# Kernel optimization log

Hardware: AMD Instinct MI355X
Metric: run time of the kernel (lower is better)

## Reference

```python
import jax, jax.numpy as jnp
import numpy as np

IMAGE_SIZE = 1024      # config.model.image_size
DOWNSIZING = 64        # PromptGetter default grid downsizing
THRESHOLD = 0.65       # default_threshold_target
NEG = -1e9             # stand-in for -inf that keeps argmax well-defined


def setup_inputs() -> dict:
    key = jax.random.key(0)
    k1, k2 = jax.random.split(key)
    image_embeddings = jax.random.normal(k1, (1, 256, 64, 64), dtype=jnp.float32)
    reference_feats = jax.random.normal(k2, (64, 1, 256), dtype=jnp.float32)
    # reference feats are L2-normalized masked features in the original pipeline
    reference_feats = reference_feats / jnp.linalg.norm(reference_feats, axis=-1, keepdims=True)
    return {"image_embeddings": image_embeddings,
            "reference_feats": reference_feats,
            "num_bg_points": 1}


def reference(image_embeddings, reference_feats, num_bg_points):
    # image_embeddings: (1, C, Hf, Wf); reference_feats: (L, 1, C)
    emb = image_embeddings[0]                                   # (C, Hf, Wf)
    emb = emb / jnp.linalg.norm(emb, axis=0, keepdims=True)     # channel-wise L2 norm
    # cosine similarity: (L, C) x (C, Hf, Wf) -> (L, Hf, Wf)
    sim = jnp.einsum('lc,chw->lhw', reference_feats[:, 0, :], emb)
    L = sim.shape[0]
    # postprocess_masks: bilinear upsample to image_size; original_size == image_size
    # so the crop + second resize are identities.
    sim_up = jax.image.resize(sim, (L, IMAGE_SIZE, IMAGE_SIZE), method='bilinear')

    # --- per-grid top-1 foreground point selection (fixed-shape equivalent of
    # the original where/unique/matched_matrix logic, ratio == 1 here) ---
    ng = IMAGE_SIZE // DOWNSIZING                               # 16 grids per side
    blocks = sim_up.reshape(L, ng, DOWNSIZING, ng, DOWNSIZING)
    blocks = blocks.transpose(0, 1, 3, 2, 4).reshape(L, ng * ng, DOWNSIZING * DOWNSIZING)
    masked = jnp.where(blocks > THRESHOLD, blocks, NEG)
    best = masked.max(axis=-1)                                  # (L, ng*ng)
    idx = masked.argmax(axis=-1)                                # in-block flat index
    valid = best > NEG / 2                                      # grid had any pixel > threshold
    gy, gx = jnp.divmod(jnp.arange(ng * ng), ng)                # grid row/col
    y = gy[None, :] * DOWNSIZING + idx // DOWNSIZING
    x = gx[None, :] * DOWNSIZING + idx % DOWNSIZING
    pts = jnp.stack([jnp.where(valid, x, 0).astype(jnp.float32),
                     jnp.where(valid, y, 0).astype(jnp.float32),
                     jnp.where(valid, best, 0.0)], axis=-1)     # (L, ng*ng, 3): x, y, score
    # sort by score descending (padded/invalid grids sink to the end)
    order = jnp.argsort(-pts[..., 2], axis=-1)
    pts = jnp.take_along_axis(pts, order[..., None], axis=1)

    # --- background points: num_bg_points lowest-similarity pixels ---
    flat = sim_up.reshape(L, -1)
    _, bg_idx = jax.lax.top_k(-flat, num_bg_points)             # smallest values
    bg = jnp.stack([(bg_idx % IMAGE_SIZE).astype(jnp.float32),   # x (col)
                    (bg_idx // IMAGE_SIZE).astype(jnp.float32)], # y (row)
                   axis=-1)                                      # (L, num_bg_points, 2)
    return pts, bg
```

## Files before the change

kernel.cpp:

```cpp
#include <hip/hip_runtime.h>
#include <float.h>
#include <math.h>

#define CCH 256
#define PIX 4096
#define LREF 64
#define IMGSZ 1024
#define THRESH 0.65f
#define NEGV -1.0e9f

__device__ __forceinline__ unsigned mono32(float v) {
    unsigned u = __float_as_uint(v);
    return u ^ ((unsigned)((int)u >> 31) | 0x80000000u);
}
__device__ __forceinline__ float unmono32(unsigned m) {
    unsigned u = (m & 0x80000000u) ? (m ^ 0x80000000u) : ~m;
    return __uint_as_float(u);
}
__device__ __forceinline__ float lrp(float a, float b, float w) {
    return fmaf(w, b, fmaf(-w, a, a));
}

__global__ __launch_bounds__(256) void k_sim(const float* __restrict__ emb,
                                             const float* __restrict__ ref,
                                             float* __restrict__ sim) {
    const int p  = blockIdx.x * 256 + threadIdx.x;
    const int l0 = blockIdx.y * 4;
    const float* r0 = ref + (size_t)(l0 + 0) * CCH;
    const float* r1 = ref + (size_t)(l0 + 1) * CCH;
    const float* r2 = ref + (size_t)(l0 + 2) * CCH;
    const float* r3 = ref + (size_t)(l0 + 3) * CCH;
    float a0 = 0.f, a1 = 0.f, a2 = 0.f, a3 = 0.f, nn = 0.f;
#pragma unroll 8
    for (int c = 0; c < CCH; ++c) {
        float v = emb[c * PIX + p];
        nn = fmaf(v, v, nn);
        a0 = fmaf(r0[c], v, a0);
        a1 = fmaf(r1[c], v, a1);
        a2 = fmaf(r2[c], v, a2);
        a3 = fmaf(r3[c], v, a3);
    }
    float inv = 1.0f / sqrtf(nn);
    sim[(size_t)(l0 + 0) * PIX + p] = a0 * inv;
    sim[(size_t)(l0 + 1) * PIX + p] = a1 * inv;
    sim[(size_t)(l0 + 2) * PIX + p] = a2 * inv;
    sim[(size_t)(l0 + 3) * PIX + p] = a3 * inv;
}

__global__ __launch_bounds__(256) void k_blocks(const float* __restrict__ sim,
                                                unsigned long long* __restrict__ fgk,
                                                unsigned long long* __restrict__ bgk) {
    const int gq = blockIdx.x;
    const int gy = blockIdx.y;
    const int l  = blockIdx.z;
    const int t  = threadIdx.x;

    __shared__ float patch[6][18];
    __shared__ unsigned long long s_fg[4][4];
    __shared__ unsigned long long s_bg[4];

    if (t < 108) {
        int i = t / 18, j = t % 18;
        int ry = min(max(4 * gy - 1 + i, 0), 63);
        int rx = min(max(16 * gq - 1 + j, 0), 63);
        patch[i][j] = sim[(size_t)l * PIX + ry * 64 + rx];
    }
    __syncthreads();

    const int dx = t & 63;
    const int s  = t >> 6;
    const int jb = 16 * gq - 1;
    const bool edgeB = (gy == 0  && s == 0);
    const bool edgeT = (gy == 15 && s == 3);
    const float w0 = edgeB ? 1.0f : 0.53125f;
    const float w1 = edgeB ? 1.0f : 0.96875f;
    const float w2 = edgeT ? 0.0f : 0.03125f;
    const float w3 = edgeT ? 0.0f : 0.46875f;
    const int ybase = gy * 64 + s * 16;

    unsigned long long bg = 0xFFFFFFFFFFFFFFFFULL;

#pragma unroll
    for (int c = 0; c < 4; ++c) {
        int x = gq * 256 + c * 64 + dx;
        float tx = fminf(fmaxf((float)x * 0.0625f - 0.46875f, 0.f), 63.f);
        int x0 = (int)tx; float wx = tx - (float)x0; int x1 = min(x0 + 1, 63);
        int j0 = x0 - jb, j1 = x1 - jb;
        float hA = lrp(patch[s    ][j0], patch[s    ][j1], wx);
        float hB = lrp(patch[s + 1][j0], patch[s + 1][j1], wx);
        float hC = lrp(patch[s + 2][j0], patch[s + 2][j1], wx);
        float e0 = lrp(hA, hB, w0);
        float e1 = lrp(hA, hB, w1);
        float e2 = lrp(hB, hC, w2);
        float e3 = lrp(hB, hC, w3);
        float bv = e0; int bk = 0;
        if (e1 < bv) { bv = e1; bk = 7; }
        if (e2 < bv) { bv = e2; bk = 8; }
        if (e3 < bv) { bv = e3; bk = 15; }
        unsigned long long key = ((unsigned long long)mono32(bv) << 32)
                               | (unsigned)(((ybase + bk) << 10) + x);
        if (key < bg) bg = key;
        unsigned long long fk = 0ULL;
        if (__ballot(fmaxf(fmaxf(e0, e1), fmaxf(e2, e3)) > THRESH)) {
            float gv = e0; int gk = 0;
            if (e1 > gv) { gv = e1; gk = 7; }
            if (e2 > gv) { gv = e2; gk = 8; }
            if (e3 > gv) { gv = e3; gk = 15; }
            int fi = (s * 16 + gk) * 64 + dx;
            fk = (gv > THRESH)
               ? (((unsigned long long)mono32(gv) << 32) | (unsigned)(4095 - fi))
               : 0ULL;
#pragma unroll
            for (int off = 32; off > 0; off >>= 1) {
                unsigned long long o = __shfl_xor(fk, off);
                if (o > fk) fk = o;
            }
        }
        if ((t & 63) == 0) s_fg[c][s] = fk;
    }

#pragma unroll
    for (int off = 32; off > 0; off >>= 1) {
        unsigned long long o = __shfl_xor(bg, off);
        if (o < bg) bg = o;
    }
    if ((t & 63) == 0) s_bg[s] = bg;
    __syncthreads();
    if (t == 0) {
        unsigned long long g = s_bg[0];
#pragma unroll
        for (int w = 1; w < 4; ++w) if (s_bg[w] < g) g = s_bg[w];
        int cell0 = (l * 16 + gy) * 16 + 4 * gq;
#pragma unroll
        for (int c = 0; c < 4; ++c) {
            unsigned long long a = s_fg[c][0];
            if (s_fg[c][1] > a) a = s_fg[c][1];
            if (s_fg[c][2] > a) a = s_fg[c][2];
            if (s_fg[c][3] > a) a = s_fg[c][3];
            fgk[cell0 + c] = a;
            bgk[cell0 + c] = g;
        }
    }
}

__global__ __launch_bounds__(256) void k_final(const unsigned long long* __restrict__ fgk,
                                               const unsigned long long* __restrict__ bgk,
                                               float* __restrict__ out) {
    const int l = blockIdx.x;
    const int t = threadIdx.x;

    __shared__ float sc[256];
    __shared__ unsigned long long s_bg[4];

    unsigned long long key = fgk[l * 256 + t];
    bool valid = key != 0ULL;
    float val = unmono32((unsigned)(key >> 32));
    int   fi  = 4095 - (int)(key & 0xFFFFFFFFULL);
    int gy = t >> 4, gx = t & 15;
    float xx = valid ? (float)(gx * 64 + (fi & 63)) : 0.f;
    float yy = valid ? (float)(gy * 64 + (fi >> 6)) : 0.f;
    float ss = valid ? val : 0.f;

    sc[t] = ss;
    unsigned long long bg = bgk[l * 256 + t];
    __syncthreads();

    int rank = 0;
    for (int j = 0; j < 256; ++j) {
        float o = sc[j];
        rank += (o > ss) || (o == ss && j < t);
    }
    float* p = out + (size_t)(l * 256 + rank) * 3;
    p[0] = xx; p[1] = yy; p[2] = ss;

#pragma unroll
    for (int off = 32; off > 0; off >>= 1) {
        unsigned long long o = __shfl_xor(bg, off);
        if (o < bg) bg = o;
    }
    if ((t & 63) == 0) s_bg[t >> 6] = bg;
    __syncthreads();
    if (t == 0) {
#pragma unroll
        for (int w = 1; w < 4; ++w) if (s_bg[w] < bg) bg = s_bg[w];
        unsigned idx = (unsigned)(bg & 0xFFFFFFFFULL);
        out[(size_t)LREF * 256 * 3 + l * 2 + 0] = (float)(idx & (IMGSZ - 1));
        out[(size_t)LREF * 256 * 3 + l * 2 + 1] = (float)(idx >> 10);
    }
}

extern "C" void kernel_launch(void* const* d_in, const int* in_sizes, int n_in,
                              void* d_out, int out_size, void* d_ws, size_t ws_size,
                              hipStream_t stream) {
    const float* emb = (const float*)d_in[0];
    const float* ref = (const float*)d_in[1];
    float* out = (float*)d_out;

    float* ws = (float*)d_ws;
    float* sim = ws;
    unsigned long long* fgk = (unsigned long long*)(sim + (size_t)LREF * PIX);
    unsigned long long* bgk = fgk + (size_t)LREF * 256;

    k_sim<<<dim3(PIX / 256, LREF / 4), dim3(256), 0, stream>>>(emb, ref, sim);
    k_blocks<<<dim3(4, 16, LREF), dim3(256), 0, stream>>>(sim, fgk, bgk);
    k_final<<<dim3(LREF), dim3(256), 0, stream>>>(fgk, bgk, out);
}
```

Before: 86.16 us.

## Fuse similarity computation into block upsample kernel, recomputing halo patches

Merges the similarity kernel and the per-grid upsample/argmax kernel into one launch. Each block computes the cosine similarity only for the 6x34 low-res halo patch it needs for 4 references, keeping it in shared memory instead of writing and re-reading a global sim buffer. Each wave now handles one reference across 8 grid columns and does its reductions with wave shuffles, so the final shared-memory combine is gone. In exchange, halo pixels are recomputed by neighbouring blocks, only 204 of 256 threads do the 256-channel dot product, and the grid shrinks to 512 blocks, which may leave the GPU underused.

```diff
diff --git a/kernel.cpp b/kernel.cpp
--- a/kernel.cpp
+++ b/kernel.cpp
@@ -7,7 +7,8 @@
 #define LREF 64
 #define IMGSZ 1024
 #define THRESH 0.65f
-#define NEGV -1.0e9f
+
+typedef unsigned long long u64;
 
 __device__ __forceinline__ unsigned mono32(float v) {
     unsigned u = __float_as_uint(v);
@@ -21,138 +22,124 @@
     return fmaf(w, b, fmaf(-w, a, a));
 }
 
-__global__ __launch_bounds__(256) void k_sim(const float* __restrict__ emb,
-                                             const float* __restrict__ ref,
-                                             float* __restrict__ sim) {
-    const int p  = blockIdx.x * 256 + threadIdx.x;
-    const int l0 = blockIdx.y * 4;
-    const float* r0 = ref + (size_t)(l0 + 0) * CCH;
-    const float* r1 = ref + (size_t)(l0 + 1) * CCH;
-    const float* r2 = ref + (size_t)(l0 + 2) * CCH;
-    const float* r3 = ref + (size_t)(l0 + 3) * CCH;
-    float a0 = 0.f, a1 = 0.f, a2 = 0.f, a3 = 0.f, nn = 0.f;
-#pragma unroll 8
-    for (int c = 0; c < CCH; ++c) {
-        float v = emb[c * PIX + p];
-        nn = fmaf(v, v, nn);
-        a0 = fmaf(r0[c], v, a0);
-        a1 = fmaf(r1[c], v, a1);
-        a2 = fmaf(r2[c], v, a2);
-        a3 = fmaf(r3[c], v, a3);
-    }
-    float inv = 1.0f / sqrtf(nn);
-    sim[(size_t)(l0 + 0) * PIX + p] = a0 * inv;
-    sim[(size_t)(l0 + 1) * PIX + p] = a1 * inv;
-    sim[(size_t)(l0 + 2) * PIX + p] = a2 * inv;
-    sim[(size_t)(l0 + 3) * PIX + p] = a3 * inv;
-}
-
-__global__ __launch_bounds__(256) void k_blocks(const float* __restrict__ sim,
-                                                unsigned long long* __restrict__ fgk,
-                                                unsigned long long* __restrict__ bgk) {
-    const int gq = blockIdx.x;
-    const int gy = blockIdx.y;
-    const int l  = blockIdx.z;
+__global__ __launch_bounds__(256) void k_fused(const float* __restrict__ emb,
+                                               const float* __restrict__ ref,
+                                               u64* __restrict__ fgk,
+                                               u64* __restrict__ bgk) {
+    const int gy = blockIdx.x;
+    const int lg = blockIdx.y;
+    const int z  = blockIdx.z;
     const int t  = threadIdx.x;
 
-    __shared__ float patch[6][18];
-    __shared__ unsigned long long s_fg[4][4];
-    __shared__ unsigned long long s_bg[4];
+    __shared__ float patch[4][6][34];
 
-    if (t < 108) {
-        int i = t / 18, j = t % 18;
-        int ry = min(max(4 * gy - 1 + i, 0), 63);
-        int rx = min(max(16 * gq - 1 + j, 0), 63);
-        patch[i][j] = sim[(size_t)l * PIX + ry * 64 + rx];
+    const int jb = 32 * z - 1;
+    const float* r0 = ref + (size_t)(lg * 4 + 0) * CCH;
+    const float* r1 = ref + (size_t)(lg * 4 + 1) * CCH;
+    const float* r2 = ref + (size_t)(lg * 4 + 2) * CCH;
+    const float* r3 = ref + (size_t)(lg * 4 + 3) * CCH;
+
+    if (t < 204) {
+        int ri = t / 34, j = t % 34;
+        int rr = min(max(4 * gy - 1 + ri, 0), 63);
+        int cc = min(max(jb + j, 0), 63);
+        const float* ep = emb + rr * 64 + cc;
+        float a0 = 0.f, a1 = 0.f, a2 = 0.f, a3 = 0.f, nn = 0.f;
+#pragma unroll 8
+        for (int c = 0; c < CCH; ++c) {
+            float v = ep[(size_t)c * PIX];
+            nn = fmaf(v, v, nn);
+            a0 = fmaf(r0[c], v, a0);
+            a1 = fmaf(r1[c], v, a1);
+            a2 = fmaf(r2[c], v, a2);
+            a3 = fmaf(r3[c], v, a3);
+        }
+        float inv = 1.0f / sqrtf(nn);
+        patch[0][ri][j] = a0 * inv;
+        patch[1][ri][j] = a1 * inv;
+        patch[2][ri][j] = a2 * inv;
+        patch[3][ri][j] = a3 * inv;
     }
     __syncthreads();
 
-    const int dx = t & 63;
-    const int s  = t >> 6;
-    const int jb = 16 * gq - 1;
-    const bool edgeB = (gy == 0  && s == 0);
-    const bool edgeT = (gy == 15 && s == 3);
-    const float w0 = edgeB ? 1.0f : 0.53125f;
-    const float w1 = edgeB ? 1.0f : 0.96875f;
-    const float w2 = edgeT ? 0.0f : 0.03125f;
-    const float w3 = edgeT ? 0.0f : 0.46875f;
-    const int ybase = gy * 64 + s * 16;
+    const int dx  = t & 63;
+    const int l2  = t >> 6;
+    const int l   = lg * 4 + l2;
+    const bool gy0 = (gy == 0), gy15 = (gy == 15);
 
-    unsigned long long bg = 0xFFFFFFFFFFFFFFFFULL;
-
-#pragma unroll
-    for (int c = 0; c < 4; ++c) {
-        int x = gq * 256 + c * 64 + dx;
+    for (int ci = 0; ci < 8; ++ci) {
+        int cxg = 8 * z + ci;
+        int x = cxg * 64 + dx;
         float tx = fminf(fmaxf((float)x * 0.0625f - 0.46875f, 0.f), 63.f);
         int x0 = (int)tx; float wx = tx - (float)x0; int x1 = min(x0 + 1, 63);
         int j0 = x0 - jb, j1 = x1 - jb;
-        float hA = lrp(patch[s    ][j0], patch[s    ][j1], wx);
-        float hB = lrp(patch[s + 1][j0], patch[s + 1][j1], wx);
-        float hC = lrp(patch[s + 2][j0], patch[s + 2][j1], wx);
-        float e0 = lrp(hA, hB, w0);
-        float e1 = lrp(hA, hB, w1);
-        float e2 = lrp(hB, hC, w2);
-        float e3 = lrp(hB, hC, w3);
-        float bv = e0; int bk = 0;
-        if (e1 < bv) { bv = e1; bk = 7; }
-        if (e2 < bv) { bv = e2; bk = 8; }
-        if (e3 < bv) { bv = e3; bk = 15; }
-        unsigned long long key = ((unsigned long long)mono32(bv) << 32)
-                               | (unsigned)(((ybase + bk) << 10) + x);
-        if (key < bg) bg = key;
-        unsigned long long fk = 0ULL;
-        if (__ballot(fmaxf(fmaxf(e0, e1), fmaxf(e2, e3)) > THRESH)) {
-            float gv = e0; int gk = 0;
-            if (e1 > gv) { gv = e1; gk = 7; }
-            if (e2 > gv) { gv = e2; gk = 8; }
-            if (e3 > gv) { gv = e3; gk = 15; }
-            int fi = (s * 16 + gk) * 64 + dx;
-            fk = (gv > THRESH)
-               ? (((unsigned long long)mono32(gv) << 32) | (unsigned)(4095 - fi))
-               : 0ULL;
+
+        u64 bg = 0xFFFFFFFFFFFFFFFFULL;
+        u64 fg = 0ULL;
+#pragma unroll
+        for (int s = 0; s < 4; ++s) {
+            float hA = lrp(patch[l2][s    ][j0], patch[l2][s    ][j1], wx);
+            float hB = lrp(patch[l2][s + 1][j0], patch[l2][s + 1][j1], wx);
+            float hC = lrp(patch[l2][s + 2][j0], patch[l2][s + 2][j1], wx);
+            bool eB = gy0  && (s == 0);
+            bool eT = gy15 && (s == 3);
+            float w0 = eB ? 1.0f : 0.53125f;
+            float w1 = eB ? 1.0f : 0.96875f;
+            float w2 = eT ? 0.0f : 0.03125f;
+            float w3 = eT ? 0.0f : 0.46875f;
+            float e0 = lrp(hA, hB, w0);
+            float e1 = lrp(hA, hB, w1);
+            float e2 = lrp(hB, hC, w2);
+            float e3 = lrp(hB, hC, w3);
+            float bv = e0; int bk = 0;
+            if (e1 < bv) { bv = e1; bk = 7; }
+            if (e2 < bv) { bv = e2; bk = 8; }
+            if (e3 < bv) { bv = e3; bk = 15; }
+            u64 key = ((u64)mono32(bv) << 32)
+                    | (unsigned)(((gy * 64 + s * 16 + bk) << 10) + x);
+            if (key < bg) bg = key;
+            if (__ballot(fmaxf(fmaxf(e0, e1), fmaxf(e2, e3)) > THRESH)) {
+                float gv = e0; int gk = 0;
+                if (e1 > gv) { gv = e1; gk = 7; }
+                if (e2 > gv) { gv = e2; gk = 8; }
+                if (e3 > gv) { gv = e3; gk = 15; }
+                int fi = (s * 16 + gk) * 64 + dx;
+                u64 fk = (gv > THRESH)
+                       ? (((u64)mono32(gv) << 32) | (unsigned)(4095 - fi))
+                       : 0ULL;
+                if (fk > fg) fg = fk;
+            }
+        }
+#pragma unroll
+        for (int off = 32; off > 0; off >>= 1) {
+            u64 o = __shfl_xor(bg, off);
+            if (o < bg) bg = o;
+        }
+        if (__ballot(fg != 0ULL)) {
 #pragma unroll
             for (int off = 32; off > 0; off >>= 1) {
-                unsigned long long o = __shfl_xor(fk, off);
-                if (o > fk) fk = o;
+                u64 o = __shfl_xor(fg, off);
+                if (o > fg) fg = o;
             }
         }
-        if ((t & 63) == 0) s_fg[c][s] = fk;
-    }
-
-#pragma unroll
-    for (int off = 32; off > 0; off >>= 1) {
-        unsigned long long o = __shfl_xor(bg, off);
-        if (o < bg) bg = o;
-    }
-    if ((t & 63) == 0) s_bg[s] = bg;
-    __syncthreads();
-    if (t == 0) {
-        unsigned long long g = s_bg[0];
-#pragma unroll
-        for (int w = 1; w < 4; ++w) if (s_bg[w] < g) g = s_bg[w];
-        int cell0 = (l * 16 + gy) * 16 + 4 * gq;
-#pragma unroll
-        for (int c = 0; c < 4; ++c) {
-            unsigned long long a = s_fg[c][0];
-            if (s_fg[c][1] > a) a = s_fg[c][1];
-            if (s_fg[c][2] > a) a = s_fg[c][2];
-            if (s_fg[c][3] > a) a = s_fg[c][3];
-            fgk[cell0 + c] = a;
-            bgk[cell0 + c] = g;
+        if (dx == 0) {
+            int cell = (l * 16 + gy) * 16 + cxg;
+            bgk[cell] = bg;
+            fgk[cell] = fg;
         }
     }
 }
 
-__global__ __launch_bounds__(256) void k_final(const unsigned long long* __restrict__ fgk,
-                                               const unsigned long long* __restrict__ bgk,
+__global__ __launch_bounds__(256) void k_final(const u64* __restrict__ fgk,
+                                               const u64* __restrict__ bgk,
                                                float* __restrict__ out) {
     const int l = blockIdx.x;
     const int t = threadIdx.x;
 
     __shared__ float sc[256];
-    __shared__ unsigned long long s_bg[4];
+    __shared__ u64 s_bg[4];
 
-    unsigned long long key = fgk[l * 256 + t];
+    u64 key = fgk[l * 256 + t];
     bool valid = key != 0ULL;
     float val = unmono32((unsigned)(key >> 32));
     int   fi  = 4095 - (int)(key & 0xFFFFFFFFULL);
@@ -162,7 +149,7 @@
     float ss = valid ? val : 0.f;
 
     sc[t] = ss;
-    unsigned long long bg = bgk[l * 256 + t];
+    u64 bg = bgk[l * 256 + t];
     __syncthreads();
 
     int rank = 0;
@@ -175,7 +162,7 @@
 
 #pragma unroll
     for (int off = 32; off > 0; off >>= 1) {
-        unsigned long long o = __shfl_xor(bg, off);
+        u64 o = __shfl_xor(bg, off);
         if (o < bg) bg = o;
     }
     if ((t & 63) == 0) s_bg[t >> 6] = bg;
@@ -196,12 +183,9 @@
     const float* ref = (const float*)d_in[1];
     float* out = (float*)d_out;
 
-    float* ws = (float*)d_ws;
-    float* sim = ws;
-    unsigned long long* fgk = (unsigned long long*)(sim + (size_t)LREF * PIX);
-    unsigned long long* bgk = fgk + (size_t)LREF * 256;
+    u64* fgk = (u64*)d_ws;
+    u64* bgk = fgk + (size_t)LREF * 256;
 
-    k_sim<<<dim3(PIX / 256, LREF / 4), dim3(256), 0, stream>>>(emb, ref, sim);
-    k_blocks<<<dim3(4, 16, LREF), dim3(256), 0, stream>>>(sim, fgk, bgk);
+    k_fused<<<dim3(16, 16, 2), dim3(256), 0, stream>>>(emb, ref, fgk, bgk);
     k_final<<<dim3(LREF), dim3(256), 0, stream>>>(fgk, bgk, out);
 }
```

Result: no change. 85.56 us (-0.7%).
